# Optimization experiments

Hardware: AMD Instinct MI355X
Metric: run time of the kernel (lower is better)

Reference implementation:

```python
import jax, jax.numpy as jnp
import numpy as np

N_NODES, D_H, D_MSG, N_LAYERS = 512, 64, 64, 3
T, E = 128, 8192


def setup_inputs() -> dict:
    key = jax.random.key(0)
    ks = jax.random.split(key, 16)
    s = 0.1
    t = jax.random.uniform(ks[0], (T,), dtype=jnp.float32)
    edge_index = jax.random.randint(ks[1], (2, E), 0, N_NODES, dtype=jnp.int64)
    inp = {
        "t": t,
        "edge_index": edge_index,
        "enc_w": jax.random.normal(ks[2], (1 + N_NODES, D_H), jnp.float32) * s,
        "enc_b": jnp.zeros((D_H,), jnp.float32),
        "msg1_w": jax.random.normal(ks[3], (N_LAYERS, 2 * D_H, D_MSG), jnp.float32) * s,
        "msg1_b": jnp.zeros((N_LAYERS, D_MSG), jnp.float32),
        "msg2_w": jax.random.normal(ks[4], (N_LAYERS, D_MSG, D_MSG), jnp.float32) * s,
        "msg2_b": jnp.zeros((N_LAYERS, D_MSG), jnp.float32),
        "upd1_w": jax.random.normal(ks[5], (N_LAYERS, D_H + D_MSG, D_H), jnp.float32) * s,
        "upd1_b": jnp.zeros((N_LAYERS, D_H), jnp.float32),
        "upd2_w": jax.random.normal(ks[6], (N_LAYERS, D_H, D_H), jnp.float32) * s,
        "upd2_b": jnp.zeros((N_LAYERS, D_H), jnp.float32),
        "ro_w": jax.random.normal(ks[7], (D_H, 1), jnp.float32) * s,
        "ro_b": jnp.zeros((1,), jnp.float32),
    }
    return inp


def reference(t, edge_index, enc_w, enc_b, msg1_w, msg1_b, msg2_w, msg2_b,
              upd1_w, upd1_b, upd2_w, upd2_b, ro_w, ro_b):
    Tn = t.shape[0]
    N = enc_w.shape[0] - 1
    L = msg1_w.shape[0]
    # node features: [t, one_hot(node_id)] -> encode
    t_feat = jnp.broadcast_to(t[:, None, None], (Tn, N, 1))          # [T,N,1]
    id_feat = jnp.broadcast_to(jnp.eye(N, dtype=t.dtype), (Tn, N, N))  # [T,N,N]
    x = jnp.concatenate([t_feat, id_feat], axis=-1)                   # [T,N,1+N]
    h = x @ enc_w + enc_b                                             # [T,N,d_h]
    src, dst = edge_index[0], edge_index[1]
    for l in range(L):
        # message MLP on gathered [h_src, h_dst]
        cat = jnp.concatenate([h[:, src], h[:, dst]], axis=-1)        # [T,E,2*d_h]
        m = jax.nn.silu(cat @ msg1_w[l] + msg1_b[l]) @ msg2_w[l] + msg2_b[l]  # [T,E,d_msg]
        # scatter-add into destination nodes (index_add)
        agg = jnp.zeros((Tn, N, m.shape[-1]), dtype=h.dtype).at[:, dst].add(m)
        u = jnp.concatenate([h, agg], axis=-1)                        # [T,N,d_h+d_msg]
        upd = jax.nn.silu(u @ upd1_w[l] + upd1_b[l]) @ upd2_w[l] + upd2_b[l]
        h = h + upd                                                   # residual
    out = (h @ ro_w + ro_b)[..., 0]                                   # [T,N]
    return out
```

## Files before the change

### kernel.cpp

```cpp
#include <hip/hip_runtime.h>

#define TT 128
#define NN 512
#define DH 64
#define EE 8192
#define LOB (18 * 8 * 64)

typedef __bf16 bf16x8 __attribute__((ext_vector_type(8)));
typedef float f32x4 __attribute__((ext_vector_type(4)));

struct US8 { unsigned short u[8]; };
struct Frag { bf16x8 hi, lo; };

static __device__ __forceinline__ unsigned short f2bf(float x) {
    union { float f; unsigned u; } c; c.f = x;
    unsigned r = (c.u + 0x7FFFu + ((c.u >> 16) & 1u)) >> 16;
    return (unsigned short)r;
}
static __device__ __forceinline__ float bf2f(unsigned short b) {
    union { unsigned u; float f; } c; c.u = ((unsigned)b) << 16;
    return c.f;
}
static __device__ __forceinline__ float silu_acc(float a, float b, float acc) {
    float x = a + b;
    float e = __expf(-x);
    return fmaf(x, __builtin_amdgcn_rcpf(1.0f + e), acc);
}
static __device__ __forceinline__ float silu_f(float x) {
    float e = __expf(-x);
    return x * __builtin_amdgcn_rcpf(1.0f + e);
}
static __device__ __forceinline__ Frag split8(const float* v) {
    Frag f;
    #pragma unroll
    for (int i = 0; i < 8; ++i) {
        __bf16 hb = (__bf16)v[i];
        f.hi[i] = hb;
        f.lo[i] = (__bf16)(v[i] - (float)hb);
    }
    return f;
}
static __device__ __forceinline__ f32x4 mmac(bf16x8 a, uint4 bw, f32x4 c) {
    return __builtin_amdgcn_mfma_f32_16x16x32_bf16(
        a, __builtin_bit_cast(bf16x8, bw), c, 0, 0, 0);
}
static __device__ __forceinline__ f32x4 mm3(Frag a, uint4 wh, uint4 wl, f32x4 c) {
    c = mmac(a.hi, wh, c);
    c = mmac(a.lo, wh, c);
    c = mmac(a.hi, wl, c);
    return c;
}

__global__ __launch_bounds__(512) void setup_kernel(
    const int* __restrict__ ei,
    const float* __restrict__ msg1_w, const float* __restrict__ msg2_w,
    const float* __restrict__ upd1_w, const float* __restrict__ upd2_w,
    uint4* __restrict__ pack,
    int* __restrict__ counts, int* __restrict__ offsets,
    int* __restrict__ ssrc) {
    int b = blockIdx.x;
    if (b < 18) {
        int l = b / 6, bi = b % 6;
        const float* W;
        if (bi == 0)      W = msg1_w + (size_t)l * 128 * 64;
        else if (bi == 1) W = msg1_w + (size_t)l * 128 * 64 + 64 * 64;
        else if (bi == 2) W = msg2_w + (size_t)l * 64 * 64;
        else if (bi == 3) W = upd1_w + (size_t)l * 128 * 64;
        else if (bi == 4) W = upd1_w + (size_t)l * 128 * 64 + 64 * 64;
        else              W = upd2_w + (size_t)l * 64 * 64;
        int lane = threadIdx.x & 63;
        int sub  = threadIdx.x >> 6;
        int nt = sub >> 1, kc = sub & 1;
        US8 oh, ol;
        #pragma unroll
        for (int i = 0; i < 8; ++i) {
            int k = kc * 32 + (lane >> 4) * 8 + i;
            int col = nt * 16 + (lane & 15);
            float w = W[k * 64 + col];
            unsigned short hu = f2bf(w);
            oh.u[i] = hu;
            ol.u[i] = f2bf(w - bf2f(hu));
        }
        size_t fi = ((size_t)b * 8 + sub) * 64 + lane;
        pack[fi]       = __builtin_bit_cast(uint4, oh);
        pack[LOB + fi] = __builtin_bit_cast(uint4, ol);
        return;
    }
    __shared__ int cnt[NN];
    __shared__ int tmp[NN];
    __shared__ int cur[NN];
    int i = threadIdx.x;
    cnt[i] = 0;
    __syncthreads();
    #pragma unroll
    for (int r = 0; r < EE / 512; ++r)
        atomicAdd(&cnt[ei[EE + r * 512 + i]], 1);
    __syncthreads();
    int c = cnt[i];
    tmp[i] = c;
    __syncthreads();
    for (int off = 1; off < NN; off <<= 1) {
        int v = (i >= off) ? tmp[i - off] : 0;
        __syncthreads();
        tmp[i] += v;
        __syncthreads();
    }
    counts[i] = c;
    offsets[i + 1] = tmp[i];
    if (i == 0) offsets[0] = 0;
    cur[i] = tmp[i] - c;
    __syncthreads();
    #pragma unroll
    for (int r = 0; r < EE / 512; ++r) {
        int e = r * 512 + i;
        int dst = ei[EE + e];
        int pos = atomicAdd(&cur[dst], 1);
        ssrc[pos] = ei[e];
    }
}

__global__ __launch_bounds__(256) void encode_mfma_kernel(
    const float* __restrict__ t, const float* __restrict__ enc_w,
    const float* __restrict__ enc_b, const float* __restrict__ b1,
    const uint4* __restrict__ pack,
    float* __restrict__ h, float* __restrict__ hs, float* __restrict__ hd) {
    int lane = threadIdx.x & 63;
    int rowbase = blockIdx.x * 64 + (threadIdx.x >> 6) * 16;
    int arow = lane & 15, kgrp = lane >> 4, k0 = kgrp * 8;
    int row = rowbase + arow;
    int tt = row >> 9, n = row & (NN - 1);
    float tv = t[tt];

    float hv[16];
    #pragma unroll
    for (int kc = 0; kc < 2; ++kc) {
        #pragma unroll
        for (int i = 0; i < 8; ++i) {
            int k = kc * 32 + k0 + i;
            hv[kc * 8 + i] = tv * enc_w[k] + enc_w[(1 + n) * DH + k] + enc_b[k];
        }
        *(float4*)(h + (size_t)row * DH + kc * 32 + k0) =
            make_float4(hv[kc * 8], hv[kc * 8 + 1], hv[kc * 8 + 2], hv[kc * 8 + 3]);
        *(float4*)(h + (size_t)row * DH + kc * 32 + k0 + 4) =
            make_float4(hv[kc * 8 + 4], hv[kc * 8 + 5], hv[kc * 8 + 6], hv[kc * 8 + 7]);
    }
    Frag a0 = split8(&hv[0]), a1 = split8(&hv[8]);

    const uint4* PWtH = pack;
    const uint4* PWbH = pack + 8 * 64;
    const uint4* PWtL = PWtH + LOB;
    const uint4* PWbL = PWbH + LOB;
    #pragma unroll
    for (int nt = 0; nt < 4; ++nt) {
        f32x4 s; f32x4 d;
        float b1v = b1[nt * 16 + (lane & 15)];
        #pragma unroll
        for (int r = 0; r < 4; ++r) { s[r] = 0.f; d[r] = b1v; }
        s = mm3(a0, PWtH[(nt * 2 + 0) * 64 + lane], PWtL[(nt * 2 + 0) * 64 + lane], s);
        s = mm3(a1, PWtH[(nt * 2 + 1) * 64 + lane], PWtL[(nt * 2 + 1) * 64 + lane], s);
        d = mm3(a0, PWbH[(nt * 2 + 0) * 64 + lane], PWbL[(nt * 2 + 0) * 64 + lane], d);
        d = mm3(a1, PWbH[(nt * 2 + 1) * 64 + lane], PWbL[(nt * 2 + 1) * 64 + lane], d);
        #pragma unroll
        for (int r = 0; r < 4; ++r) {
            int rr = rowbase + kgrp * 4 + r;
            hs[(size_t)rr * DH + nt * 16 + (lane & 15)] = s[r];
            hd[(size_t)rr * DH + nt * 16 + (lane & 15)] = d[r];
        }
    }
}

__global__ __launch_bounds__(256) void agg_kernel(
    const float* __restrict__ hs, const float* __restrict__ hd,
    const int* __restrict__ offsets, const int* __restrict__ ssrc,
    float* __restrict__ aggpre) {
    int lane = threadIdx.x & 63;
    int n = blockIdx.x * 4 + (threadIdx.x >> 6);
    int tt = blockIdx.y;
    size_t rowoff = ((size_t)tt * NN + n) * DH;
    int eg = lane >> 4;
    int ch4 = (lane & 15) * 16;
    float4 hdv = *(const float4*)(hd + rowoff + (lane & 15) * 4);
    int beg = offsets[n], end = offsets[n + 1];
    const char* hb = (const char*)(hs + (size_t)tt * NN * DH);
    float4 acc = make_float4(0.f, 0.f, 0.f, 0.f);
    int i = beg + eg;
    for (; i + 4 < end; i += 8) {
        int s0 = ssrc[i] << 8;
        int s1 = ssrc[i + 4] << 8;
        float4 v0 = *(const float4*)(hb + s0 + ch4);
        float4 v1 = *(const float4*)(hb + s1 + ch4);
        acc.x = silu_acc(v0.x, hdv.x, acc.x);
        acc.y = silu_acc(v0.y, hdv.y, acc.y);
        acc.z = silu_acc(v0.z, hdv.z, acc.z);
        acc.w = silu_acc(v0.w, hdv.w, acc.w);
        acc.x = silu_acc(v1.x, hdv.x, acc.x);
        acc.y = silu_acc(v1.y, hdv.y, acc.y);
        acc.z = silu_acc(v1.z, hdv.z, acc.z);
        acc.w = silu_acc(v1.w, hdv.w, acc.w);
    }
    if (i < end) {
        int s0 = ssrc[i] << 8;
        float4 v0 = *(const float4*)(hb + s0 + ch4);
        acc.x = silu_acc(v0.x, hdv.x, acc.x);
        acc.y = silu_acc(v0.y, hdv.y, acc.y);
        acc.z = silu_acc(v0.z, hdv.z, acc.z);
        acc.w = silu_acc(v0.w, hdv.w, acc.w);
    }
    acc.x += __shfl_xor(acc.x, 16); acc.x += __shfl_xor(acc.x, 32);
    acc.y += __shfl_xor(acc.y, 16); acc.y += __shfl_xor(acc.y, 32);
    acc.z += __shfl_xor(acc.z, 16); acc.z += __shfl_xor(acc.z, 32);
    acc.w += __shfl_xor(acc.w, 16); acc.w += __shfl_xor(acc.w, 32);
    if (eg == 0) *(float4*)(aggpre + rowoff + (lane & 15) * 4) = acc;
}

__global__ __launch_bounds__(256) void upd_mfma_kernel(
    float* __restrict__ h, const float* __restrict__ aggpre,
    const int* __restrict__ counts, const uint4* __restrict__ pack, int l,
    const float* __restrict__ b2, const float* __restrict__ ub1,
    const float* __restrict__ ub2, const float* __restrict__ b1n,
    float* __restrict__ hs, float* __restrict__ hd,
    const float* __restrict__ ro_w, const float* __restrict__ ro_b,
    float* __restrict__ out, int last) {
    __shared__ float tileA[4][16 * 68];
    __shared__ float tileB[4][16 * 68];
    int lane = threadIdx.x & 63;
    int w = threadIdx.x >> 6;
    int rowbase = blockIdx.x * 64 + w * 16;
    float* TA = tileA[w];
    float* TB = tileB[w];
    int arow = lane & 15, kgrp = lane >> 4, k0 = kgrp * 8;
    int hrow = rowbase + arow;

    float hf[16];
    *(float4*)&hf[0]  = *(const float4*)(h + (size_t)hrow * DH + k0);
    *(float4*)&hf[4]  = *(const float4*)(h + (size_t)hrow * DH + k0 + 4);
    *(float4*)&hf[8]  = *(const float4*)(h + (size_t)hrow * DH + 32 + k0);
    *(float4*)&hf[12] = *(const float4*)(h + (size_t)hrow * DH + 32 + k0 + 4);
    Frag ha0 = split8(&hf[0]), ha1 = split8(&hf[8]);

    float gf[16];
    *(float4*)&gf[0]  = *(const float4*)(aggpre + (size_t)hrow * DH + k0);
    *(float4*)&gf[4]  = *(const float4*)(aggpre + (size_t)hrow * DH + k0 + 4);
    *(float4*)&gf[8]  = *(const float4*)(aggpre + (size_t)hrow * DH + 32 + k0);
    *(float4*)&gf[12] = *(const float4*)(aggpre + (size_t)hrow * DH + 32 + k0 + 4);
    Frag ga0 = split8(&gf[0]), ga1 = split8(&gf[8]);

    const uint4* PW2H = pack + (size_t)(l * 6 + 2) * 8 * 64;
    const uint4* PW2L = PW2H + LOB;
    float degv[4];
    #pragma unroll
    for (int r = 0; r < 4; ++r)
        degv[r] = (float)counts[(rowbase + kgrp * 4 + r) & (NN - 1)];
    #pragma unroll
    for (int nt = 0; nt < 4; ++nt) {
        float b2v = b2[nt * 16 + (lane & 15)];
        f32x4 a;
        #pragma unroll
        for (int r = 0; r < 4; ++r) a[r] = degv[r] * b2v;
        a = mm3(ga0, PW2H[(nt * 2 + 0) * 64 + lane], PW2L[(nt * 2 + 0) * 64 + lane], a);
        a = mm3(ga1, PW2H[(nt * 2 + 1) * 64 + lane], PW2L[(nt * 2 + 1) * 64 + lane], a);
        #pragma unroll
        for (int r = 0; r < 4; ++r)
            TA[(kgrp * 4 + r) * 68 + nt * 16 + (lane & 15)] = a[r];
    }
    float za[16];
    #pragma unroll
    for (int i = 0; i < 8; ++i) za[i] = TA[arow * 68 + k0 + i];
    #pragma unroll
    for (int i = 0; i < 8; ++i) za[8 + i] = TA[arow * 68 + 32 + k0 + i];
    Frag ka0 = split8(&za[0]), ka1 = split8(&za[8]);

    const uint4* PU1tH = pack + (size_t)(l * 6 + 3) * 8 * 64;
    const uint4* PU1bH = pack + (size_t)(l * 6 + 4) * 8 * 64;
    const uint4* PU1tL = PU1tH + LOB;
    const uint4* PU1bL = PU1bH + LOB;
    #pragma unroll
    for (int nt = 0; nt < 4; ++nt) {
        float bv = ub1[nt * 16 + (lane & 15)];
        f32x4 a;
        #pragma unroll
        for (int r = 0; r < 4; ++r) a[r] = bv;
        a = mm3(ha0, PU1tH[(nt * 2 + 0) * 64 + lane], PU1tL[(nt * 2 + 0) * 64 + lane], a);
        a = mm3(ha1, PU1tH[(nt * 2 + 1) * 64 + lane], PU1tL[(nt * 2 + 1) * 64 + lane], a);
        a = mm3(ka0, PU1bH[(nt * 2 + 0) * 64 + lane], PU1bL[(nt * 2 + 0) * 64 + lane], a);
        a = mm3(ka1, PU1bH[(nt * 2 + 1) * 64 + lane], PU1bL[(nt * 2 + 1) * 64 + lane], a);
        #pragma unroll
        for (int r = 0; r < 4; ++r)
            TB[(kgrp * 4 + r) * 68 + nt * 16 + (lane & 15)] = silu_f(a[r]);
    }
    float zb[16];
    #pragma unroll
    for (int i = 0; i < 8; ++i) zb[i] = TB[arow * 68 + k0 + i];
    #pragma unroll
    for (int i = 0; i < 8; ++i) zb[8 + i] = TB[arow * 68 + 32 + k0 + i];
    Frag kz0 = split8(&zb[0]), kz1 = split8(&zb[8]);

    const uint4* PU2H = pack + (size_t)(l * 6 + 5) * 8 * 64;
    const uint4* PU2L = PU2H + LOB;
    #pragma unroll
    for (int nt = 0; nt < 4; ++nt) {
        float bv = ub2[nt * 16 + (lane & 15)];
        f32x4 a;
        #pragma unroll
        for (int r = 0; r < 4; ++r) a[r] = bv;
        a = mm3(kz0, PU2H[(nt * 2 + 0) * 64 + lane], PU2L[(nt * 2 + 0) * 64 + lane], a);
        a = mm3(kz1, PU2H[(nt * 2 + 1) * 64 + lane], PU2L[(nt * 2 + 1) * 64 + lane], a);
        #pragma unroll
        for (int r = 0; r < 4; ++r)
            TA[(kgrp * 4 + r) * 68 + nt * 16 + (lane & 15)] = a[r];
    }
    float hn[16];
    #pragma unroll
    for (int i = 0; i < 8; ++i) hn[i] = hf[i] + TA[arow * 68 + k0 + i];
    #pragma unroll
    for (int i = 0; i < 8; ++i) hn[8 + i] = hf[8 + i] + TA[arow * 68 + 32 + k0 + i];

    if (last) {
        float v = 0.f;
        #pragma unroll
        for (int i = 0; i < 8; ++i) v += hn[i] * ro_w[k0 + i];
        #pragma unroll
        for (int i = 0; i < 8; ++i) v += hn[8 + i] * ro_w[32 + k0 + i];
        v += __shfl_xor(v, 16);
        v += __shfl_xor(v, 32);
        if (lane < 16) out[rowbase + lane] = v + ro_b[0];
        return;
    }

    *(float4*)(h + (size_t)hrow * DH + k0) = make_float4(hn[0], hn[1], hn[2], hn[3]);
    *(float4*)(h + (size_t)hrow * DH + k0 + 4) = make_float4(hn[4], hn[5], hn[6], hn[7]);
    *(float4*)(h + (size_t)hrow * DH + 32 + k0) = make_float4(hn[8], hn[9], hn[10], hn[11]);
    *(float4*)(h + (size_t)hrow * DH + 32 + k0 + 4) = make_float4(hn[12], hn[13], hn[14], hn[15]);

    Frag na0 = split8(&hn[0]), na1 = split8(&hn[8]);
    const uint4* PWtH = pack + (size_t)((l + 1) * 6 + 0) * 8 * 64;
    const uint4* PWbH = pack + (size_t)((l + 1) * 6 + 1) * 8 * 64;
    const uint4* PWtL = PWtH + LOB;
    const uint4* PWbL = PWbH + LOB;
    #pragma unroll
    for (int nt = 0; nt < 4; ++nt) {
        f32x4 s; f32x4 d;
        float b1v = b1n[nt * 16 + (lane & 15)];
        #pragma unroll
        for (int r = 0; r < 4; ++r) { s[r] = 0.f; d[r] = b1v; }
        s = mm3(na0, PWtH[(nt * 2 + 0) * 64 + lane], PWtL[(nt * 2 + 0) * 64 + lane], s);
        s = mm3(na1, PWtH[(nt * 2 + 1) * 64 + lane], PWtL[(nt * 2 + 1) * 64 + lane], s);
        d = mm3(na0, PWbH[(nt * 2 + 0) * 64 + lane], PWbL[(nt * 2 + 0) * 64 + lane], d);
        d = mm3(na1, PWbH[(nt * 2 + 1) * 64 + lane], PWbL[(nt * 2 + 1) * 64 + lane], d);
        #pragma unroll
        for (int r = 0; r < 4; ++r) {
            int rr = rowbase + kgrp * 4 + r;
            hs[(size_t)rr * DH + nt * 16 + (lane & 15)] = s[r];
            hd[(size_t)rr * DH + nt * 16 + (lane & 15)] = d[r];
        }
    }
}

extern "C" void kernel_launch(void* const* d_in, const int* in_sizes, int n_in,
                              void* d_out, int out_size, void* d_ws, size_t ws_size,
                              hipStream_t stream) {
    const float* t      = (const float*)d_in[0];
    const int*   ei     = (const int*)d_in[1];
    const float* enc_w  = (const float*)d_in[2];
    const float* enc_b  = (const float*)d_in[3];
    const float* msg1_w = (const float*)d_in[4];
    const float* msg1_b = (const float*)d_in[5];
    const float* msg2_w = (const float*)d_in[6];
    const float* msg2_b = (const float*)d_in[7];
    const float* upd1_w = (const float*)d_in[8];
    const float* upd1_b = (const float*)d_in[9];
    const float* upd2_w = (const float*)d_in[10];
    const float* upd2_b = (const float*)d_in[11];
    const float* ro_w   = (const float*)d_in[12];
    const float* ro_b   = (const float*)d_in[13];
    float* out = (float*)d_out;

    const size_t HN = (size_t)TT * NN * DH;
    float* h      = (float*)d_ws;
    float* hs     = h + HN;
    float* hd     = hs + HN;
    float* aggpre = hd + HN;
    uint4* pack   = (uint4*)(aggpre + HN);
    int* counts  = (int*)(pack + 2 * LOB);
    int* offsets = counts + NN;
    int* ssrc    = offsets + NN + 1;

    setup_kernel<<<19, 512, 0, stream>>>(ei, msg1_w, msg2_w, upd1_w, upd2_w,
                                         pack, counts, offsets, ssrc);

    encode_mfma_kernel<<<TT * NN / 64, 256, 0, stream>>>(
        t, enc_w, enc_b, msg1_b, pack, h, hs, hd);

    for (int l = 0; l < 3; ++l) {
        agg_kernel<<<dim3(NN / 4, TT), 256, 0, stream>>>(
            hs, hd, offsets, ssrc, aggpre);
        int last = (l == 2);
        upd_mfma_kernel<<<TT * NN / 64, 256, 0, stream>>>(
            h, aggpre, counts, pack, l,
            msg2_b + (size_t)l * DH, upd1_b + (size_t)l * DH,
            upd2_b + (size_t)l * DH,
            last ? msg1_b : msg1_b + (size_t)(l + 1) * DH,
            hs, hd, ro_w, ro_b, out, last);
    }
}
```

Before: 298.6 us.

## Fuse edge aggregation into the update kernel with XCD-aware block swizzle

Removes the separate agg_kernel and computes each wave's 16-node aggregation inside the new layer_kernel, staging it in shared memory instead of writing and re-reading a global aggpre buffer. hs is ping-ponged between two buffers so blocks can write next-layer hs while others still gather the current one. A block-index swizzle puts all node tiles of the same timestep on the same XCD, so the gathered hs slice can stay in that XCD's L2. The trade-off is less parallelism in the gather phase: each wave now walks 16 nodes' edge lists one after another, where before one wave handled one node.

```diff
diff --git a/kernel.cpp b/kernel.cpp
--- a/kernel.cpp
+++ b/kernel.cpp
@@ -119,13 +119,21 @@
     }
 }
 
+static __device__ __forceinline__ int swz_rowbase(int bid, int w) {
+    int xcd = bid & 7;
+    int idx = bid >> 3;
+    int tt  = xcd * 16 + (idx >> 3);
+    int sub = idx & 7;
+    return tt * NN + sub * 64 + w * 16;
+}
+
 __global__ __launch_bounds__(256) void encode_mfma_kernel(
     const float* __restrict__ t, const float* __restrict__ enc_w,
     const float* __restrict__ enc_b, const float* __restrict__ b1,
     const uint4* __restrict__ pack,
     float* __restrict__ h, float* __restrict__ hs, float* __restrict__ hd) {
     int lane = threadIdx.x & 63;
-    int rowbase = blockIdx.x * 64 + (threadIdx.x >> 6) * 16;
+    int rowbase = swz_rowbase(blockIdx.x, threadIdx.x >> 6);
     int arow = lane & 15, kgrp = lane >> 4, k0 = kgrp * 8;
     int row = rowbase + arow;
     int tt = row >> 9, n = row & (NN - 1);
@@ -169,67 +177,70 @@
     }
 }
 
-__global__ __launch_bounds__(256) void agg_kernel(
-    const float* __restrict__ hs, const float* __restrict__ hd,
-    const int* __restrict__ offsets, const int* __restrict__ ssrc,
-    float* __restrict__ aggpre) {
-    int lane = threadIdx.x & 63;
-    int n = blockIdx.x * 4 + (threadIdx.x >> 6);
-    int tt = blockIdx.y;
-    size_t rowoff = ((size_t)tt * NN + n) * DH;
-    int eg = lane >> 4;
-    int ch4 = (lane & 15) * 16;
-    float4 hdv = *(const float4*)(hd + rowoff + (lane & 15) * 4);
-    int beg = offsets[n], end = offsets[n + 1];
-    const char* hb = (const char*)(hs + (size_t)tt * NN * DH);
-    float4 acc = make_float4(0.f, 0.f, 0.f, 0.f);
-    int i = beg + eg;
-    for (; i + 4 < end; i += 8) {
-        int s0 = ssrc[i] << 8;
-        int s1 = ssrc[i + 4] << 8;
-        float4 v0 = *(const float4*)(hb + s0 + ch4);
-        float4 v1 = *(const float4*)(hb + s1 + ch4);
-        acc.x = silu_acc(v0.x, hdv.x, acc.x);
-        acc.y = silu_acc(v0.y, hdv.y, acc.y);
-        acc.z = silu_acc(v0.z, hdv.z, acc.z);
-        acc.w = silu_acc(v0.w, hdv.w, acc.w);
-        acc.x = silu_acc(v1.x, hdv.x, acc.x);
-        acc.y = silu_acc(v1.y, hdv.y, acc.y);
-        acc.z = silu_acc(v1.z, hdv.z, acc.z);
-        acc.w = silu_acc(v1.w, hdv.w, acc.w);
-    }
-    if (i < end) {
-        int s0 = ssrc[i] << 8;
-        float4 v0 = *(const float4*)(hb + s0 + ch4);
-        acc.x = silu_acc(v0.x, hdv.x, acc.x);
-        acc.y = silu_acc(v0.y, hdv.y, acc.y);
-        acc.z = silu_acc(v0.z, hdv.z, acc.z);
-        acc.w = silu_acc(v0.w, hdv.w, acc.w);
-    }
-    acc.x += __shfl_xor(acc.x, 16); acc.x += __shfl_xor(acc.x, 32);
-    acc.y += __shfl_xor(acc.y, 16); acc.y += __shfl_xor(acc.y, 32);
-    acc.z += __shfl_xor(acc.z, 16); acc.z += __shfl_xor(acc.z, 32);
-    acc.w += __shfl_xor(acc.w, 16); acc.w += __shfl_xor(acc.w, 32);
-    if (eg == 0) *(float4*)(aggpre + rowoff + (lane & 15) * 4) = acc;
-}
-
-__global__ __launch_bounds__(256) void upd_mfma_kernel(
-    float* __restrict__ h, const float* __restrict__ aggpre,
-    const int* __restrict__ counts, const uint4* __restrict__ pack, int l,
+__global__ __launch_bounds__(256) void layer_kernel(
+    float* __restrict__ h, const float* __restrict__ hs_in,
+    float* __restrict__ hs_out, float* __restrict__ hd,
+    const int* __restrict__ counts, const int* __restrict__ offsets,
+    const int* __restrict__ ssrc, const uint4* __restrict__ pack, int l,
     const float* __restrict__ b2, const float* __restrict__ ub1,
     const float* __restrict__ ub2, const float* __restrict__ b1n,
-    float* __restrict__ hs, float* __restrict__ hd,
     const float* __restrict__ ro_w, const float* __restrict__ ro_b,
     float* __restrict__ out, int last) {
+    __shared__ float TAgg[4][16 * 68];
     __shared__ float tileA[4][16 * 68];
     __shared__ float tileB[4][16 * 68];
     int lane = threadIdx.x & 63;
     int w = threadIdx.x >> 6;
-    int rowbase = blockIdx.x * 64 + w * 16;
+    int rowbase = swz_rowbase(blockIdx.x, w);
+    int tt = rowbase >> 9;
+    int nbase = rowbase & (NN - 1);
+    float* TG = TAgg[w];
     float* TA = tileA[w];
     float* TB = tileB[w];
     int arow = lane & 15, kgrp = lane >> 4, k0 = kgrp * 8;
     int hrow = rowbase + arow;
+
+    {
+        int eg = lane >> 4;
+        int chb = (lane & 15) * 4;
+        int ch4 = chb * 4;
+        const char* hb = (const char*)(hs_in + (size_t)tt * NN * DH);
+        for (int j = 0; j < 16; ++j) {
+            int nn = nbase + j;
+            size_t rowoff = ((size_t)tt * NN + nn) * DH;
+            float4 hdv = *(const float4*)(hd + rowoff + chb);
+            int beg = offsets[nn], end = offsets[nn + 1];
+            float4 acc = make_float4(0.f, 0.f, 0.f, 0.f);
+            int i = beg + eg;
+            for (; i + 4 < end; i += 8) {
+                int s0 = ssrc[i] << 8;
+                int s1 = ssrc[i + 4] << 8;
+                float4 v0 = *(const float4*)(hb + s0 + ch4);
+                float4 v1 = *(const float4*)(hb + s1 + ch4);
+                acc.x = silu_acc(v0.x, hdv.x, acc.x);
+                acc.y = silu_acc(v0.y, hdv.y, acc.y);
+                acc.z = silu_acc(v0.z, hdv.z, acc.z);
+                acc.w = silu_acc(v0.w, hdv.w, acc.w);
+                acc.x = silu_acc(v1.x, hdv.x, acc.x);
+                acc.y = silu_acc(v1.y, hdv.y, acc.y);
+                acc.z = silu_acc(v1.z, hdv.z, acc.z);
+                acc.w = silu_acc(v1.w, hdv.w, acc.w);
+            }
+            if (i < end) {
+                int s0 = ssrc[i] << 8;
+                float4 v0 = *(const float4*)(hb + s0 + ch4);
+                acc.x = silu_acc(v0.x, hdv.x, acc.x);
+                acc.y = silu_acc(v0.y, hdv.y, acc.y);
+                acc.z = silu_acc(v0.z, hdv.z, acc.z);
+                acc.w = silu_acc(v0.w, hdv.w, acc.w);
+            }
+            acc.x += __shfl_xor(acc.x, 16); acc.x += __shfl_xor(acc.x, 32);
+            acc.y += __shfl_xor(acc.y, 16); acc.y += __shfl_xor(acc.y, 32);
+            acc.z += __shfl_xor(acc.z, 16); acc.z += __shfl_xor(acc.z, 32);
+            acc.w += __shfl_xor(acc.w, 16); acc.w += __shfl_xor(acc.w, 32);
+            if (eg == 0) *(float4*)(&TG[j * 68 + chb]) = acc;
+        }
+    }
 
     float hf[16];
     *(float4*)&hf[0]  = *(const float4*)(h + (size_t)hrow * DH + k0);
@@ -239,10 +250,10 @@
     Frag ha0 = split8(&hf[0]), ha1 = split8(&hf[8]);
 
     float gf[16];
-    *(float4*)&gf[0]  = *(const float4*)(aggpre + (size_t)hrow * DH + k0);
-    *(float4*)&gf[4]  = *(const float4*)(aggpre + (size_t)hrow * DH + k0 + 4);
-    *(float4*)&gf[8]  = *(const float4*)(aggpre + (size_t)hrow * DH + 32 + k0);
-    *(float4*)&gf[12] = *(const float4*)(aggpre + (size_t)hrow * DH + 32 + k0 + 4);
+    #pragma unroll
+    for (int i = 0; i < 8; ++i) gf[i] = TG[arow * 68 + k0 + i];
+    #pragma unroll
+    for (int i = 0; i < 8; ++i) gf[8 + i] = TG[arow * 68 + 32 + k0 + i];
     Frag ga0 = split8(&gf[0]), ga1 = split8(&gf[8]);
 
     const uint4* PW2H = pack + (size_t)(l * 6 + 2) * 8 * 64;
@@ -350,7 +361,7 @@
         #pragma unroll
         for (int r = 0; r < 4; ++r) {
             int rr = rowbase + kgrp * 4 + r;
-            hs[(size_t)rr * DH + nt * 16 + (lane & 15)] = s[r];
+            hs_out[(size_t)rr * DH + nt * 16 + (lane & 15)] = s[r];
             hd[(size_t)rr * DH + nt * 16 + (lane & 15)] = d[r];
         }
     }
@@ -376,11 +387,11 @@
     float* out = (float*)d_out;
 
     const size_t HN = (size_t)TT * NN * DH;
-    float* h      = (float*)d_ws;
-    float* hs     = h + HN;
-    float* hd     = hs + HN;
-    float* aggpre = hd + HN;
-    uint4* pack   = (uint4*)(aggpre + HN);
+    float* h    = (float*)d_ws;
+    float* hs0  = h + HN;
+    float* hs1  = hs0 + HN;
+    float* hd   = hs1 + HN;
+    uint4* pack = (uint4*)(hd + HN);
     int* counts  = (int*)(pack + 2 * LOB);
     int* offsets = counts + NN;
     int* ssrc    = offsets + NN + 1;
@@ -389,17 +400,17 @@
                                          pack, counts, offsets, ssrc);
 
     encode_mfma_kernel<<<TT * NN / 64, 256, 0, stream>>>(
-        t, enc_w, enc_b, msg1_b, pack, h, hs, hd);
-
+        t, enc_w, enc_b, msg1_b, pack, h, hs0, hd);
+
+    float* hsbuf[2] = {hs0, hs1};
     for (int l = 0; l < 3; ++l) {
-        agg_kernel<<<dim3(NN / 4, TT), 256, 0, stream>>>(
-            hs, hd, offsets, ssrc, aggpre);
         int last = (l == 2);
-        upd_mfma_kernel<<<TT * NN / 64, 256, 0, stream>>>(
-            h, aggpre, counts, pack, l,
+        layer_kernel<<<TT * NN / 64, 256, 0, stream>>>(
+            h, hsbuf[l & 1], hsbuf[(l + 1) & 1], hd,
+            counts, offsets, ssrc, pack, l,
             msg2_b + (size_t)l * DH, upd1_b + (size_t)l * DH,
             upd2_b + (size_t)l * DH,
             last ? msg1_b : msg1_b + (size_t)(l + 1) * DH,
-            hs, hd, ro_w, ro_b, out, last);
-    }
-}
+            ro_w, ro_b, out, last);
+    }
+}
```

Measured after the change: 349.7 us. +17.1%, slower.

## Swizzle block-to-row mapping so each XCD owns contiguous timesteps

Applied to the files above, without the earlier changes.

Remaps block indices in the encode, aggregation and update kernels so that blocks landing on the same XCD (round-robin by blockIdx mod 8) process a contiguous range of 16 timesteps. The aim is to keep each timestep's hs/hd gather footprint in the XCD-local L2 instead of spreading it across all eight. The update kernel also reuses a single shared tile for both intermediate stages, halving LDS use, which could raise occupancy. This relies on the hardware dispatching workgroups to XCDs round-robin.

```diff
diff --git a/kernel.cpp b/kernel.cpp
--- a/kernel.cpp
+++ b/kernel.cpp
@@ -119,13 +119,21 @@
     }
 }
 
+static __device__ __forceinline__ int swz_rowbase(int bid, int w) {
+    int xcd = bid & 7;
+    int idx = bid >> 3;
+    int tt  = xcd * 16 + (idx >> 3);
+    int sub = idx & 7;
+    return tt * NN + sub * 64 + w * 16;
+}
+
 __global__ __launch_bounds__(256) void encode_mfma_kernel(
     const float* __restrict__ t, const float* __restrict__ enc_w,
     const float* __restrict__ enc_b, const float* __restrict__ b1,
     const uint4* __restrict__ pack,
     float* __restrict__ h, float* __restrict__ hs, float* __restrict__ hd) {
     int lane = threadIdx.x & 63;
-    int rowbase = blockIdx.x * 64 + (threadIdx.x >> 6) * 16;
+    int rowbase = swz_rowbase(blockIdx.x, threadIdx.x >> 6);
     int arow = lane & 15, kgrp = lane >> 4, k0 = kgrp * 8;
     int row = rowbase + arow;
     int tt = row >> 9, n = row & (NN - 1);
@@ -173,9 +181,12 @@
     const float* __restrict__ hs, const float* __restrict__ hd,
     const int* __restrict__ offsets, const int* __restrict__ ssrc,
     float* __restrict__ aggpre) {
+    int bid = blockIdx.x;
+    int xcd = bid & 7;
+    int idx = bid >> 3;
+    int tt  = xcd * 16 + (idx >> 7);
+    int n   = (idx & 127) * 4 + (threadIdx.x >> 6);
     int lane = threadIdx.x & 63;
-    int n = blockIdx.x * 4 + (threadIdx.x >> 6);
-    int tt = blockIdx.y;
     size_t rowoff = ((size_t)tt * NN + n) * DH;
     int eg = lane >> 4;
     int ch4 = (lane & 15) * 16;
@@ -221,13 +232,11 @@
     float* __restrict__ hs, float* __restrict__ hd,
     const float* __restrict__ ro_w, const float* __restrict__ ro_b,
     float* __restrict__ out, int last) {
-    __shared__ float tileA[4][16 * 68];
-    __shared__ float tileB[4][16 * 68];
+    __shared__ float tile[4][16 * 68];
     int lane = threadIdx.x & 63;
     int w = threadIdx.x >> 6;
-    int rowbase = blockIdx.x * 64 + w * 16;
-    float* TA = tileA[w];
-    float* TB = tileB[w];
+    int rowbase = swz_rowbase(blockIdx.x, w);
+    float* TA = tile[w];
     int arow = lane & 15, kgrp = lane >> 4, k0 = kgrp * 8;
     int hrow = rowbase + arow;
 
@@ -286,13 +295,13 @@
         a = mm3(ka1, PU1bH[(nt * 2 + 1) * 64 + lane], PU1bL[(nt * 2 + 1) * 64 + lane], a);
         #pragma unroll
         for (int r = 0; r < 4; ++r)
-            TB[(kgrp * 4 + r) * 68 + nt * 16 + (lane & 15)] = silu_f(a[r]);
+            TA[(kgrp * 4 + r) * 68 + nt * 16 + (lane & 15)] = silu_f(a[r]);
     }
     float zb[16];
     #pragma unroll
-    for (int i = 0; i < 8; ++i) zb[i] = TB[arow * 68 + k0 + i];
-    #pragma unroll
-    for (int i = 0; i < 8; ++i) zb[8 + i] = TB[arow * 68 + 32 + k0 + i];
+    for (int i = 0; i < 8; ++i) zb[i] = TA[arow * 68 + k0 + i];
+    #pragma unroll
+    for (int i = 0; i < 8; ++i) zb[8 + i] = TA[arow * 68 + 32 + k0 + i];
     Frag kz0 = split8(&zb[0]), kz1 = split8(&zb[8]);
 
     const uint4* PU2H = pack + (size_t)(l * 6 + 5) * 8 * 64;
@@ -392,7 +401,7 @@
         t, enc_w, enc_b, msg1_b, pack, h, hs, hd);
 
     for (int l = 0; l < 3; ++l) {
-        agg_kernel<<<dim3(NN / 4, TT), 256, 0, stream>>>(
+        agg_kernel<<<TT * NN / 4, 256, 0, stream>>>(
             hs, hd, offsets, ssrc, aggpre);
         int last = (l == 2);
         upd_mfma_kernel<<<TT * NN / 64, 256, 0, stream>>>(
```

New measurement: 275.5 us. 7.7% less time.
